# Kernel optimization log

Hardware: AMD Instinct MI355X
Metric: run time of the kernel (lower is better)

The kernel has to match this reference:

```python
import jax, jax.numpy as jnp
import numpy as np

INPUT_SIZE = 10
HIDDEN_SIZE = 20
T, B = 512, 4096


def setup_inputs() -> dict:
    key = jax.random.key(0)
    ks = jax.random.split(key, 7)
    # PyTorch LSTMCell init: uniform(-k, k), k = 1/sqrt(hidden_size)
    k = 1.0 / np.sqrt(HIDDEN_SIZE)
    u = lambda kk, shape: jax.random.uniform(kk, shape, jnp.float32, -k, k)
    return {
        "input_sequence": jax.random.normal(ks[0], (T, B, INPUT_SIZE), jnp.float32),
        "initial_h": jax.random.normal(ks[1], (B, HIDDEN_SIZE), jnp.float32),
        "initial_c": jax.random.normal(ks[2], (B, HIDDEN_SIZE), jnp.float32),
        "W_ih": u(ks[3], (4 * HIDDEN_SIZE, INPUT_SIZE)),
        "W_hh": u(ks[4], (4 * HIDDEN_SIZE, HIDDEN_SIZE)),
        "b_ih": u(ks[5], (4 * HIDDEN_SIZE,)),
        "b_hh": u(ks[6], (4 * HIDDEN_SIZE,)),
    }


def _lstm_scan(input_sequence, initial_h, initial_c, W_ih, W_hh, b_ih, b_hh):
    H = initial_h.shape[-1]
    # Precompute input projections for all timesteps in one big GEMM:
    # [T, B, 4H] = [T, B, I] @ [I, 4H]
    x_proj = jnp.einsum("tbi,gi->tbg", input_sequence, W_ih) + b_ih + b_hh

    def step(carry, xg):
        h, c = carry
        gates = xg + h @ W_hh.T  # [B, 4H]
        i, f, g, o = jnp.split(gates, 4, axis=-1)  # PyTorch gate order i,f,g,o
        i = jax.nn.sigmoid(i)
        f = jax.nn.sigmoid(f)
        g = jnp.tanh(g)
        o = jax.nn.sigmoid(o)
        c_new = f * c + i * g
        h_new = o * jnp.tanh(c_new)
        return (h_new, c_new), h_new

    (h, c), outputs = jax.lax.scan(step, (initial_h, initial_c), x_proj)
    return outputs, h, c


def reference(input_sequence, initial_h, initial_c, W_ih, W_hh, b_ih, b_hh):
    return _lstm_scan(input_sequence, initial_h, initial_c, W_ih, W_hh, b_ih, b_hh)
```

## Files before the change

### kernel.cpp

```cpp
#include <hip/hip_runtime.h>


#define T_STEPS 512
#define BATCH   4096
#define ISZ     10
#define HSZ     20
#define BPB     3
#define PF      4
#define LDSPAD  22

typedef float v2f __attribute__((ext_vector_type(2)));

__device__ __forceinline__ v2f fma2(v2f a, v2f b, v2f c) {
    return __builtin_elementwise_fma(a, b, c);
}

#if defined(__has_builtin)
#if __has_builtin(__builtin_amdgcn_exp2f)
#define FAST_EXP2(x) __builtin_amdgcn_exp2f(x)
#endif
#if __has_builtin(__builtin_amdgcn_rcpf)
#define FAST_RCP(x) __builtin_amdgcn_rcpf(x)
#endif
#endif
#ifndef FAST_EXP2
#define FAST_EXP2(x) exp2f(x)
#endif
#ifndef FAST_RCP
#define FAST_RCP(x) (1.0f/(x))
#endif

__device__ __forceinline__ float sigm_f(float x) {
    return FAST_RCP(1.0f + FAST_EXP2(x * -1.4426950408889634f));
}
__device__ __forceinline__ float tanh_f(float x) {
    return 2.0f * FAST_RCP(1.0f + FAST_EXP2(x * -2.8853900817779268f)) - 1.0f;
}

__global__ __launch_bounds__(64, 1) void lstm_fused_kernel(
    const float* __restrict__ x,
    const float* __restrict__ h0,
    const float* __restrict__ c0,
    const float* __restrict__ Wih,
    const float* __restrict__ Whh,
    const float* __restrict__ bih,
    const float* __restrict__ bhh,
    float* __restrict__ out)
{
    __shared__ __align__(8) float hbuf[BPB][LDSPAD];

    const int tid = threadIdx.x;
    const int b   = tid / HSZ;
    const int j   = tid % HSZ;
    const int gb  = blockIdx.x * BPB + b;
    if (tid >= BPB * HSZ || gb >= BATCH) return;

    v2f wv[4][15];
    float bias[4];
#pragma unroll
    for (int r = 0; r < 4; ++r) {
        const int row = r * HSZ + j;
        const v2f* wi = (const v2f*)(Wih + row * ISZ);
        const v2f* wh = (const v2f*)(Whh + row * HSZ);
#pragma unroll
        for (int k = 0; k < 5; ++k)  wv[r][k] = wi[k];
#pragma unroll
        for (int k = 0; k < 10; ++k) wv[r][5 + k] = wh[k];
        bias[r] = bih[row] + bhh[row];
    }

    float c = c0[(size_t)gb * HSZ + j];
    hbuf[b][j] = h0[(size_t)gb * HSZ + j];

    const float* xbase = x + (size_t)gb * ISZ;
    float* outp = out + (size_t)gb * HSZ + j;

    v2f nx[PF][5];
#pragma unroll
    for (int p = 0; p < PF; ++p) {
        const v2f* xp = (const v2f*)(xbase + (size_t)p * BATCH * ISZ);
#pragma unroll
        for (int q = 0; q < 5; ++q) nx[p][q] = xp[q];
    }

    const v2f* hrow = (const v2f*)(&hbuf[b][0]);
    float hn = hbuf[b][j];

    for (int tb = 0; tb < T_STEPS; tb += PF) {
#pragma unroll
        for (int u = 0; u < PF; ++u) {
            const int t = tb + u;

            v2f hv[10];
#pragma unroll
            for (int q = 0; q < 10; ++q) hv[q] = hrow[q];

            v2f a[4];
#pragma unroll
            for (int r = 0; r < 4; ++r) {
                a[r] = (v2f){bias[r], 0.0f};
#pragma unroll
                for (int k = 0; k < 5; ++k) a[r] = fma2(wv[r][k], nx[u][k], a[r]);
            }

            {
                int tp = t + PF; if (tp > T_STEPS - 1) tp = T_STEPS - 1;
                const v2f* xp = (const v2f*)(xbase + (size_t)tp * BATCH * ISZ);
#pragma unroll
                for (int q = 0; q < 5; ++q) nx[u][q] = xp[q];
            }

#pragma unroll
            for (int r = 0; r < 4; ++r) {
#pragma unroll
                for (int k = 0; k < 10; ++k) a[r] = fma2(wv[r][5 + k], hv[k], a[r]);
            }

            const float ig = sigm_f(a[0].x + a[0].y);
            const float fg = sigm_f(a[1].x + a[1].y);
            const float gg = tanh_f(a[2].x + a[2].y);
            const float og = sigm_f(a[3].x + a[3].y);
            c  = fg * c + ig * gg;
            hn = og * tanh_f(c);

            hbuf[b][j] = hn;
            outp[(size_t)t * (BATCH * HSZ)] = hn;
        }
    }

    const size_t tail = (size_t)T_STEPS * BATCH * HSZ;
    out[tail + (size_t)gb * HSZ + j] = hn;
    out[tail + (size_t)BATCH * HSZ + (size_t)gb * HSZ + j] = c;
}

extern "C" void kernel_launch(void* const* d_in, const int* in_sizes, int n_in,
                              void* d_out, int out_size, void* d_ws, size_t ws_size,
                              hipStream_t stream) {
    const float* x   = (const float*)d_in[0];
    const float* h0  = (const float*)d_in[1];
    const float* c0  = (const float*)d_in[2];
    const float* Wih = (const float*)d_in[3];
    const float* Whh = (const float*)d_in[4];
    const float* bih = (const float*)d_in[5];
    const float* bhh = (const float*)d_in[6];
    float* out = (float*)d_out;

    const int nblk = (BATCH + BPB - 1) / BPB;
    lstm_fused_kernel<<<nblk, 64, 0, stream>>>(x, h0, c0, Wih, Whh, bih, bhh, out);
}
```

Measured before the change: 473.7 us.

## Split LSTM gates across four lanes with swizzle exchange and double-buffered LDS

Each hidden unit now uses four threads, one per gate, instead of one thread computing all four gates. Gate activations are exchanged through ds_swizzle, and blocks process four batch rows with 320 threads. The hidden state is double-buffered in LDS with a block barrier each step. This spreads the per-step FMA and transcendental work over four times as many lanes to shorten the serial recurrence critical path, at the cost of a __syncthreads per timestep, redundant loads of x and h per lane, and a prefetch depth reduced from four steps to two.

```diff
diff --git a/kernel.cpp b/kernel.cpp
--- a/kernel.cpp
+++ b/kernel.cpp
@@ -5,9 +5,8 @@
 #define BATCH   4096
 #define ISZ     10
 #define HSZ     20
-#define BPB     3
-#define PF      4
-#define LDSPAD  22
+#define GPB     4
+#define NTHR    320
 
 typedef float v2f __attribute__((ext_vector_type(2)));
 
@@ -30,14 +29,14 @@
 #define FAST_RCP(x) (1.0f/(x))
 #endif
 
-__device__ __forceinline__ float sigm_f(float x) {
-    return FAST_RCP(1.0f + FAST_EXP2(x * -1.4426950408889634f));
+template<int PAT>
+__device__ __forceinline__ float swzf(float v) {
+    return __int_as_float(__builtin_amdgcn_ds_swizzle(__float_as_int(v), PAT));
 }
-__device__ __forceinline__ float tanh_f(float x) {
-    return 2.0f * FAST_RCP(1.0f + FAST_EXP2(x * -2.8853900817779268f)) - 1.0f;
-}
+#define SWZ_XOR1 0x041F
+#define SWZ_XOR2 0x081F
 
-__global__ __launch_bounds__(64, 1) void lstm_fused_kernel(
+__global__ __launch_bounds__(NTHR, 5) void lstm_fused_kernel(
     const float* __restrict__ x,
     const float* __restrict__ h0,
     const float* __restrict__ c0,
@@ -47,90 +46,102 @@
     const float* __restrict__ bhh,
     float* __restrict__ out)
 {
-    __shared__ __align__(8) float hbuf[BPB][LDSPAD];
+    __shared__ __align__(16) float hbuf[2][GPB * HSZ];
 
     const int tid = threadIdx.x;
-    const int b   = tid / HSZ;
-    const int j   = tid % HSZ;
-    const int gb  = blockIdx.x * BPB + b;
-    if (tid >= BPB * HSZ || gb >= BATCH) return;
+    const int r   = tid & 3;
+    const int E   = tid >> 2;
+    const int bb  = E / HSZ;
+    const int j   = E - bb * HSZ;
+    const int gb  = blockIdx.x * GPB + bb;
 
-    v2f wv[4][15];
-    float bias[4];
+    const float Bc = (r == 2) ? -2.8853900817779268f : -1.4426950408889634f;
+    const float Ac = (r == 2) ? 2.0f : 1.0f;
+    const float Cc = (r == 2) ? -1.0f : 0.0f;
+
+    const int row = r * HSZ + j;
+    v2f wi[5], wh[10];
+    {
+        const v2f* wip = (const v2f*)(Wih + row * ISZ);
+        const v2f* whp = (const v2f*)(Whh + row * HSZ);
 #pragma unroll
-    for (int r = 0; r < 4; ++r) {
-        const int row = r * HSZ + j;
-        const v2f* wi = (const v2f*)(Wih + row * ISZ);
-        const v2f* wh = (const v2f*)(Whh + row * HSZ);
+        for (int k = 0; k < 5; ++k)  wi[k] = wip[k];
 #pragma unroll
-        for (int k = 0; k < 5; ++k)  wv[r][k] = wi[k];
-#pragma unroll
-        for (int k = 0; k < 10; ++k) wv[r][5 + k] = wh[k];
-        bias[r] = bih[row] + bhh[row];
+        for (int k = 0; k < 10; ++k) wh[k] = whp[k];
     }
+    const float bias = bih[row] + bhh[row];
 
     float c = c0[(size_t)gb * HSZ + j];
-    hbuf[b][j] = h0[(size_t)gb * HSZ + j];
+    if (r == 0) hbuf[0][E] = h0[(size_t)gb * HSZ + j];
 
     const float* xbase = x + (size_t)gb * ISZ;
     float* outp = out + (size_t)gb * HSZ + j;
 
-    v2f nx[PF][5];
+    v2f nxA[5], nxB[5];
+    {
+        const v2f* x0p = (const v2f*)(xbase);
+        const v2f* x1p = (const v2f*)(xbase + (size_t)BATCH * ISZ);
 #pragma unroll
-    for (int p = 0; p < PF; ++p) {
-        const v2f* xp = (const v2f*)(xbase + (size_t)p * BATCH * ISZ);
-#pragma unroll
-        for (int q = 0; q < 5; ++q) nx[p][q] = xp[q];
+        for (int q = 0; q < 5; ++q) { nxA[q] = x0p[q]; nxB[q] = x1p[q]; }
     }
 
-    const v2f* hrow = (const v2f*)(&hbuf[b][0]);
-    float hn = hbuf[b][j];
+    __syncthreads();
 
-    for (int tb = 0; tb < T_STEPS; tb += PF) {
-#pragma unroll
-        for (int u = 0; u < PF; ++u) {
-            const int t = tb + u;
+    float hn = 0.0f;
+    int cur = 0;
 
-            v2f hv[10];
-#pragma unroll
-            for (int q = 0; q < 10; ++q) hv[q] = hrow[q];
-
-            v2f a[4];
-#pragma unroll
-            for (int r = 0; r < 4; ++r) {
-                a[r] = (v2f){bias[r], 0.0f};
-#pragma unroll
-                for (int k = 0; k < 5; ++k) a[r] = fma2(wv[r][k], nx[u][k], a[r]);
-            }
-
-            {
-                int tp = t + PF; if (tp > T_STEPS - 1) tp = T_STEPS - 1;
-                const v2f* xp = (const v2f*)(xbase + (size_t)tp * BATCH * ISZ);
-#pragma unroll
-                for (int q = 0; q < 5; ++q) nx[u][q] = xp[q];
-            }
-
-#pragma unroll
-            for (int r = 0; r < 4; ++r) {
-#pragma unroll
-                for (int k = 0; k < 10; ++k) a[r] = fma2(wv[r][5 + k], hv[k], a[r]);
-            }
-
-            const float ig = sigm_f(a[0].x + a[0].y);
-            const float fg = sigm_f(a[1].x + a[1].y);
-            const float gg = tanh_f(a[2].x + a[2].y);
-            const float og = sigm_f(a[3].x + a[3].y);
-            c  = fg * c + ig * gg;
-            hn = og * tanh_f(c);
-
-            hbuf[b][j] = hn;
-            outp[(size_t)t * (BATCH * HSZ)] = hn;
-        }
+#define STEP(NX, TI)                                                          \
+    {                                                                         \
+         \
+        const v2f* hrow = (const v2f*)(&hbuf[cur][bb * HSZ]);                 \
+        v2f hv[10];                                                           \
+        _Pragma("unroll")                                                     \
+        for (int q = 0; q < 10; ++q) hv[q] = hrow[q];                         \
+                  \
+        v2f a = {bias, 0.0f};                                                 \
+        _Pragma("unroll")                                                     \
+        for (int k = 0; k < 5; ++k) a = fma2(wi[k], NX[k], a);                \
+                     \
+        {                                                                     \
+            int tp = (TI) + 2; if (tp > T_STEPS - 1) tp = T_STEPS - 1;        \
+            const v2f* xp = (const v2f*)(xbase + (size_t)tp * (BATCH*ISZ));   \
+            _Pragma("unroll")                                                 \
+            for (int q = 0; q < 5; ++q) NX[q] = xp[q];                        \
+        }                                                                     \
+                                                          \
+        _Pragma("unroll")                                                     \
+        for (int k = 0; k < 10; ++k) a = fma2(wh[k], hv[k], a);               \
+        const float g   = a.x + a.y;                                          \
+               \
+        const float act = Ac * FAST_RCP(1.0f + FAST_EXP2(g * Bc)) + Cc;       \
+            \
+        const float p1 = swzf<SWZ_XOR1>(act);                                 \
+        const float q0 = swzf<SWZ_XOR2>(act);                                 \
+        const float q1 = swzf<SWZ_XOR2>(p1);                                  \
+                  \
+        c = __builtin_fmaf(p1, c, act * q0);                                  \
+        const float th = 2.0f * FAST_RCP(1.0f +                               \
+                         FAST_EXP2(c * -2.8853900817779268f)) - 1.0f;         \
+        hn = q1 * th;                                                         \
+        if (r == 0) {                                                         \
+            hbuf[cur ^ 1][E] = hn;                   \
+            outp[(size_t)(TI) * (BATCH * HSZ)] = hn;                          \
+        }                                                                     \
+        __syncthreads();                                                      \
+        cur ^= 1;                                                             \
     }
 
-    const size_t tail = (size_t)T_STEPS * BATCH * HSZ;
-    out[tail + (size_t)gb * HSZ + j] = hn;
-    out[tail + (size_t)BATCH * HSZ + (size_t)gb * HSZ + j] = c;
+    for (int t = 0; t < T_STEPS; t += 2) {
+        STEP(nxA, t)
+        STEP(nxB, t + 1)
+    }
+#undef STEP
+
+    if (r == 0) {
+        const size_t tail = (size_t)T_STEPS * BATCH * HSZ;
+        out[tail + (size_t)gb * HSZ + j] = hn;
+        out[tail + (size_t)BATCH * HSZ + (size_t)gb * HSZ + j] = c;
+    }
 }
 
 extern "C" void kernel_launch(void* const* d_in, const int* in_sizes, int n_in,
@@ -145,6 +156,6 @@
     const float* bhh = (const float*)d_in[6];
     float* out = (float*)d_out;
 
-    const int nblk = (BATCH + BPB - 1) / BPB;
-    lstm_fused_kernel<<<nblk, 64, 0, stream>>>(x, h0, c0, Wih, Whh, bih, bhh, out);
+    const int nblk = BATCH / GPB;
+    lstm_fused_kernel<<<nblk, NTHR, 0, stream>>>(x, h0, c0, Wih, Whh, bih, bhh, out);
 }
```

Measured after the change: 654.5 us. 1.38x slower.
